# Optimization experiments

Measured on AMD Instinct MI355X. Metric: run time of the kernel, lower is better.

The kernel has to match this reference:

```python
import jax, jax.numpy as jnp
import numpy as np

EMB, HEADS = 1024, 16
B, T = 4, 1024

def setup_inputs() -> dict:
    key = jax.random.key(0)
    ks = jax.random.split(key, 6)
    sc = 1.0 / np.sqrt(EMB)
    return {
        "x": jax.random.normal(ks[0], (B, T, EMB), jnp.float32),
        "Wq": jax.random.normal(ks[1], (EMB, EMB), jnp.float32) * sc,
        "Wk": jax.random.normal(ks[2], (EMB, EMB), jnp.float32) * sc,
        "Wv": jax.random.normal(ks[3], (EMB, EMB), jnp.float32) * sc,
        "Wo": jax.random.normal(ks[4], (EMB, EMB), jnp.float32) * sc,
        "bo": jnp.zeros((EMB,), jnp.float32),
    }

def reference(x, Wq, Wk, Wv, Wo, bo):
    b, t, e = x.shape
    h = HEADS
    s = e // h
    # nn.Linear(emb, emb, bias=False): y = x @ W.T
    q = (x @ Wq.T).reshape(b, t, h, s).transpose(0, 2, 1, 3)  # (b,h,t,s)
    k = (x @ Wk.T).reshape(b, t, h, s).transpose(0, 2, 1, 3)
    v = (x @ Wv.T).reshape(b, t, h, s).transpose(0, 2, 1, 3)
    scale = e ** 0.25  # original scales q and k each by emb**(1/4)
    q = q / scale
    k = k / scale
    dot = jnp.einsum('bhqs,bhks->bhqk', q, k)  # (b,h,t,t)
    # causal mask: strict upper triangle -> -inf (mask_diagonal=False)
    causal = jnp.tril(jnp.ones((t, t), dtype=bool))
    dot = jnp.where(causal[None, None], dot, -jnp.inf)
    attn = jax.nn.softmax(dot, axis=-1)
    out = jnp.einsum('bhqk,bhks->bhqs', attn, v)  # (b,h,t,s)
    out = out.transpose(0, 2, 1, 3).reshape(b, t, e)
    return out @ Wo.T + bo
```

## Files before the change

### kernel.cpp

```cpp
#include <hip/hip_runtime.h>
#include <hip/hip_bf16.h>
#include <stdint.h>


typedef __attribute__((ext_vector_type(8))) short short8;
typedef __attribute__((ext_vector_type(4))) float f32x4;
typedef __attribute__((ext_vector_type(16))) float f32x16;

__device__ __forceinline__ unsigned short f2bf(float f) {
    union { float f; unsigned int u; } v; v.f = f;
    unsigned int r = v.u + 0x7FFFu + ((v.u >> 16) & 1u);
    return (unsigned short)(r >> 16);
}

__device__ __forceinline__ void gload_lds16(const ushort* g, ushort* l) {
    __builtin_amdgcn_global_load_lds(
        (const __attribute__((address_space(1))) void*)g,
        (__attribute__((address_space(3))) void*)l,
        16, 0, 0);
}

__device__ __forceinline__ void wait_vmcnt_0() { asm volatile("s_waitcnt vmcnt(0)" ::: "memory"); }
__device__ __forceinline__ void wait_vmcnt_3() { asm volatile("s_waitcnt vmcnt(3)" ::: "memory"); }
__device__ __forceinline__ void wait_vmcnt_4() { asm volatile("s_waitcnt vmcnt(4)" ::: "memory"); }

__device__ __forceinline__ void block_barrier() {
    __builtin_amdgcn_sched_barrier(0);
    __builtin_amdgcn_s_barrier();
    __builtin_amdgcn_sched_barrier(0);
}
__device__ __forceinline__ void lgk0() {
    asm volatile("s_waitcnt lgkmcnt(0)" ::: "memory");
    __builtin_amdgcn_sched_barrier(0);
}

__device__ __forceinline__ unsigned int cvtpk(float lo, float hi) {
    unsigned int r;
    asm("v_cvt_pk_bf16_f32 %0, %1, %2" : "=v"(r) : "v"(lo), "v"(hi));
    return r;
}
__device__ __forceinline__ void plswap(unsigned int& x, unsigned int& y) {
    asm volatile("v_permlane32_swap_b32 %0, %1" : "+v"(x), "+v"(y));
}

__global__ __launch_bounds__(256) void cast_bf16(
    const float* __restrict__ x,  const float* __restrict__ wq,
    const float* __restrict__ wk, const float* __restrict__ wv,
    const float* __restrict__ wo, ushort* __restrict__ dst)
{
    size_t e0 = (size_t)(blockIdx.x * 256 + threadIdx.x) * 4;
    const float* src; size_t off;
    if      (e0 < 4194304u) { src = x;  off = e0; }
    else if (e0 < 5242880u) { src = wq; off = e0 - 4194304u; }
    else if (e0 < 6291456u) { src = wk; off = e0 - 5242880u; }
    else if (e0 < 7340032u) { src = wv; off = e0 - 6291456u; }
    else                    { src = wo; off = e0 - 7340032u; }
    float4 v = *(const float4*)(src + off);
    ushort4 o;
    o.x = f2bf(v.x); o.y = f2bf(v.y); o.z = f2bf(v.z); o.w = f2bf(v.w);
    *(ushort4*)(dst + e0) = o;
}

__global__ __launch_bounds__(512) void gemm_qkv_8ph(
    const ushort* __restrict__ A, const ushort* __restrict__ B,
    ushort* __restrict__ Qb, ushort* __restrict__ Kb, ushort* __restrict__ Vtb)
{
    __shared__ ushort lds[2][2][2][128 * 64];

    const int id = blockIdx.x;
    const int swz = (id & 7) * 24 + (id >> 3);
    const int bx = swz % 12, by = swz / 12;
    const int n0 = bx * 256, m0 = by * 256;
    const int t = threadIdx.x, w = t >> 6, l = t & 63;
    const int l15 = l & 15, l4 = l >> 4;
    const int wr = w >> 2, wc = w & 3;
    const int K = 1024;

    auto stage_half = [&](const ushort* gsrc, ushort* dst) {
        #pragma unroll
        for (int i = 0; i < 2; ++i) {
            int slot = i * 512 + t;
            int r = slot >> 3, blk = slot & 7;
            gload_lds16(gsrc + (size_t)r * K + ((blk ^ (r & 7)) << 3),
                        dst + (i * 512 + w * 64) * 8);
        }
    };
    auto stageA = [&](int kt, int h, int buf) {
        stage_half(A + (size_t)(m0 + h * 128) * K + kt * 64, &lds[buf][0][h][0]);
    };
    auto stageB = [&](int kt, int h, int buf) {
        stage_half(B + (size_t)(n0 + h * 128) * K + kt * 64, &lds[buf][1][h][0]);
    };

    short8 af[8];
    short8 vb0[4], vb1[4];
    f32x4 acc[8][4] = {};

    auto readA = [&](int buf, int qm) {
        const ushort* base = &lds[buf][0][wr][0];
        #pragma unroll
        for (int kk = 0; kk < 2; ++kk)
            #pragma unroll
            for (int mt = 0; mt < 4; ++mt) {
                int row = qm * 64 + mt * 16 + l15;
                af[kk * 4 + mt] = *(const short8*)
                    &base[row * 64 + (((kk * 4 + l4) ^ (row & 7)) << 3)];
            }
    };
    auto readB0 = [&](int buf, int qn) {
        const ushort* base = &lds[buf][1][wc >> 1][0];
        #pragma unroll
        for (int kk = 0; kk < 2; ++kk)
            #pragma unroll
            for (int nt = 0; nt < 2; ++nt) {
                int row = (wc & 1) * 64 + qn * 32 + nt * 16 + l15;
                vb0[kk * 2 + nt] = *(const short8*)
                    &base[row * 64 + (((kk * 4 + l4) ^ (row & 7)) << 3)];
            }
    };
    auto readB1 = [&](int buf, int qn) {
        const ushort* base = &lds[buf][1][wc >> 1][0];
        #pragma unroll
        for (int kk = 0; kk < 2; ++kk)
            #pragma unroll
            for (int nt = 0; nt < 2; ++nt) {
                int row = (wc & 1) * 64 + qn * 32 + nt * 16 + l15;
                vb1[kk * 2 + nt] = *(const short8*)
                    &base[row * 64 + (((kk * 4 + l4) ^ (row & 7)) << 3)];
            }
    };
    auto mfma_vb0 = [&](int qm, int qn) {
        __builtin_amdgcn_s_setprio(1);
        #pragma unroll
        for (int kk = 0; kk < 2; ++kk)
            #pragma unroll
            for (int mt = 0; mt < 4; ++mt)
                #pragma unroll
                for (int nt = 0; nt < 2; ++nt)
                    acc[qm * 4 + mt][qn * 2 + nt] =
                        __builtin_amdgcn_mfma_f32_16x16x32_bf16(
                            af[kk * 4 + mt], vb0[kk * 2 + nt],
                            acc[qm * 4 + mt][qn * 2 + nt], 0, 0, 0);
        __builtin_amdgcn_s_setprio(0);
    };
    auto mfma_vb1 = [&](int qm, int qn) {
        __builtin_amdgcn_s_setprio(1);
        #pragma unroll
        for (int kk = 0; kk < 2; ++kk)
            #pragma unroll
            for (int mt = 0; mt < 4; ++mt)
                #pragma unroll
                for (int nt = 0; nt < 2; ++nt)
                    acc[qm * 4 + mt][qn * 2 + nt] =
                        __builtin_amdgcn_mfma_f32_16x16x32_bf16(
                            af[kk * 4 + mt], vb1[kk * 2 + nt],
                            acc[qm * 4 + mt][qn * 2 + nt], 0, 0, 0);
        __builtin_amdgcn_s_setprio(0);
    };

    stageB(0, 0, 0); stageB(0, 1, 0); stageA(0, 0, 0); stageA(0, 1, 0);
    stageB(1, 0, 1); stageB(1, 1, 1);
    wait_vmcnt_4();
    block_barrier();

    for (int j = 0; j < 8; ++j) {
        const bool more = (j < 7);
        readA(0, 0); readB0(0, 0);
        stageA(2 * j + 1, 0, 1);
        block_barrier(); lgk0();
        mfma_vb0(0, 0);
        block_barrier();
        readB1(0, 1);
        stageA(2 * j + 1, 1, 1);
        block_barrier(); lgk0();
        mfma_vb1(0, 1);
        block_barrier();
        readA(0, 1);
        if (more) stageB(2 * j + 2, 0, 0);
        block_barrier(); lgk0();
        mfma_vb1(1, 1);
        block_barrier();
        if (more) stageB(2 * j + 2, 1, 0);
        block_barrier(); lgk0();
        mfma_vb0(1, 0);
        if (more) wait_vmcnt_4(); else wait_vmcnt_0();
        block_barrier();
        readA(1, 0); readB0(1, 0);
        if (more) stageA(2 * j + 2, 0, 0);
        block_barrier(); lgk0();
        mfma_vb0(0, 0);
        block_barrier();
        readB1(1, 1);
        if (more) stageA(2 * j + 2, 1, 0);
        block_barrier(); lgk0();
        mfma_vb1(0, 1);
        block_barrier();
        readA(1, 1);
        if (more) stageB(2 * j + 3, 0, 1);
        block_barrier(); lgk0();
        mfma_vb1(1, 1);
        block_barrier();
        if (more) stageB(2 * j + 3, 1, 1);
        block_barrier(); lgk0();
        mfma_vb0(1, 0);
        if (more) { wait_vmcnt_4(); block_barrier(); }
    }

    #pragma unroll
    for (int qm = 0; qm < 2; ++qm) {
        #pragma unroll
        for (int mt = 0; mt < 4; ++mt) {
            int row = m0 + wr * 128 + qm * 64 + mt * 16 + l4 * 4;
            int b = row >> 10, tq = row & 1023;
            #pragma unroll
            for (int qn = 0; qn < 2; ++qn) {
                #pragma unroll
                for (int nt = 0; nt < 2; ++nt) {
                    int col = n0 + wc * 64 + qn * 32 + nt * 16 + l15;
                    int sel = col >> 10;
                    int cw  = col & 1023;
                    int h = cw >> 6, s = cw & 63;
                    f32x4 v = acc[qm * 4 + mt][qn * 2 + nt];
                    if (sel == 2) {
                        ushort4 o;
                        o.x = f2bf(v[0]); o.y = f2bf(v[1]);
                        o.z = f2bf(v[2]); o.w = f2bf(v[3]);
                        *(ushort4*)&Vtb[(((size_t)(b * 16 + h)) * 64 + s) * 1024 + tq] = o;
                    } else {
                        ushort* dst = (sel == 0) ? Qb : Kb;
                        float scl = (sel == 0) ? 0.03125f : 1.0f;
                        #pragma unroll
                        for (int jj = 0; jj < 4; ++jj)
                            dst[(((size_t)(b * 16 + h)) * 1024 + tq + jj) * 64 + s] =
                                f2bf(v[jj] * scl);
                    }
                }
            }
        }
    }
}

template<int MODE, int BM, int WRg, int WCg>
__global__ __launch_bounds__(256) void gemm_bt(
    const ushort* __restrict__ A, const ushort* __restrict__ B,
    float* __restrict__ Cout, const float* __restrict__ bias)
{
    constexpr int MF = BM / (32 * WRg);
    constexpr int NF = 128 / (32 * WCg);
    constexpr int NSTEP = 32;
    const int K = 1024;
    const int n0 = blockIdx.x * 128;
    const int m0 = blockIdx.y * BM;
    const int t  = threadIdx.x;
    const int w  = t >> 6, l = t & 63;
    const int l31 = l & 31, lh = l >> 5;
    const int wr = w / WCg, wc = w % WCg;

    __shared__ ushort As[3 * BM * 32];
    __shared__ ushort Bs[3 * 128 * 32];

    auto stage = [&](int j) {
        const int buf = j % 3;
        const int k0 = j * 32;
        #pragma unroll
        for (int i = 0; i < BM / 64; ++i) {
            int slot = i * 256 + t;
            int r = slot >> 2, blk = slot & 3;
            gload_lds16(A + (size_t)(m0 + r) * K + k0 + ((blk ^ ((r >> 1) & 3)) << 3),
                        &As[buf * BM * 32 + (i * 256 + w * 64) * 8]);
        }
        #pragma unroll
        for (int i = 0; i < 2; ++i) {
            int slot = i * 256 + t;
            int r = slot >> 2, blk = slot & 3;
            gload_lds16(B + (size_t)(n0 + r) * K + k0 + ((blk ^ ((r >> 1) & 3)) << 3),
                        &Bs[buf * 128 * 32 + (i * 256 + w * 64) * 8]);
        }
    };

    f32x16 acc[MF][NF] = {};

    stage(0); stage(1);
    for (int kt = 0; kt < NSTEP; ++kt) {
        if (kt < NSTEP - 1) { if (BM == 128) wait_vmcnt_4(); else wait_vmcnt_3(); }
        else wait_vmcnt_0();
        block_barrier();
        if (kt + 2 < NSTEP) stage(kt + 2);

        const ushort* Ab = &As[(kt % 3) * BM * 32];
        const ushort* Bb = &Bs[(kt % 3) * 128 * 32];
        #pragma unroll
        for (int kk = 0; kk < 2; ++kk) {
            const int c = kk * 2 + lh;
            short8 af[MF], bf[NF];
            #pragma unroll
            for (int mt = 0; mt < MF; ++mt) {
                int row = wr * (MF * 32) + mt * 32 + l31;
                af[mt] = *(const short8*)&Ab[row * 32 + ((c ^ ((row >> 1) & 3)) << 3)];
            }
            #pragma unroll
            for (int nt = 0; nt < NF; ++nt) {
                int row = wc * (NF * 32) + nt * 32 + l31;
                bf[nt] = *(const short8*)&Bb[row * 32 + ((c ^ ((row >> 1) & 3)) << 3)];
            }
            #pragma unroll
            for (int mt = 0; mt < MF; ++mt)
                #pragma unroll
                for (int nt = 0; nt < NF; ++nt)
                    acc[mt][nt] = __builtin_amdgcn_mfma_f32_32x32x16_bf16(
                        af[mt], bf[nt], acc[mt][nt], 0, 0, 0);
        }
    }

    #pragma unroll
    for (int mt = 0; mt < MF; ++mt) {
        int rbase = m0 + wr * (MF * 32) + mt * 32 + 4 * lh;
        #pragma unroll
        for (int nt = 0; nt < NF; ++nt) {
            int col = n0 + wc * (NF * 32) + nt * 32 + l31;
            float bi = bias[col];
            #pragma unroll
            for (int reg = 0; reg < 16; ++reg) {
                int row = rbase + (reg & 3) + 8 * (reg >> 2);
                Cout[(size_t)row * 1024 + col] = acc[mt][nt][reg] + bi;
            }
        }
    }
}

#define PVSTEP(SF, B, VK0, VK1)                                               \
    {                                                                         \
        unsigned int A0_ = cvtpk(SF[(B) + 0], SF[(B) + 1]);                   \
        unsigned int A1_ = cvtpk(SF[(B) + 2], SF[(B) + 3]);                   \
        unsigned int B0_ = cvtpk(SF[(B) + 4], SF[(B) + 5]);                   \
        unsigned int B1_ = cvtpk(SF[(B) + 6], SF[(B) + 7]);                   \
        plswap(A0_, B0_);                                                     \
        plswap(A1_, B1_);                                                     \
        union { unsigned int u[4]; short8 s; } pa_;                           \
        pa_.u[0] = A0_; pa_.u[1] = A1_; pa_.u[2] = B0_; pa_.u[3] = B1_;       \
        accO0 = __builtin_amdgcn_mfma_f32_32x32x16_bf16(pa_.s, VK0, accO0, 0, 0, 0); \
        accO1 = __builtin_amdgcn_mfma_f32_32x32x16_bf16(pa_.s, VK1, accO1, 0, 0, 0); \
    }

#define EXP4(SF, R)                                                           \
    SF[(R) + 0] = __expf(SF[(R) + 0]); ls0 += SF[(R) + 0];                    \
    SF[(R) + 1] = __expf(SF[(R) + 1]); ls1 += SF[(R) + 1];                    \
    SF[(R) + 2] = __expf(SF[(R) + 2]); ls2 += SF[(R) + 2];                    \
    SF[(R) + 3] = __expf(SF[(R) + 3]); ls3 += SF[(R) + 3];

#define MEXP1(SF, R, OFF, LS)                                                 \
    {                                                                         \
        int kv_ = (OFF) + ((R) & 3) + 8 * ((R) >> 2) + 4 * hi;                \
        float e_ = (kv_ > qrow) ? 0.f : __expf(SF[R]);                        \
        SF[R] = e_; LS += e_;                                                 \
    }

#define MEXP16(SF, OFF)                                                       \
    MEXP1(SF, 0, OFF, ls0)  MEXP1(SF, 1, OFF, ls1)                            \
    MEXP1(SF, 2, OFF, ls2)  MEXP1(SF, 3, OFF, ls3)                            \
    MEXP1(SF, 4, OFF, ls0)  MEXP1(SF, 5, OFF, ls1)                            \
    MEXP1(SF, 6, OFF, ls2)  MEXP1(SF, 7, OFF, ls3)                            \
    MEXP1(SF, 8, OFF, ls0)  MEXP1(SF, 9, OFF, ls1)                            \
    MEXP1(SF, 10, OFF, ls2) MEXP1(SF, 11, OFF, ls3)                           \
    MEXP1(SF, 12, OFF, ls0) MEXP1(SF, 13, OFF, ls1)                           \
    MEXP1(SF, 14, OFF, ls2) MEXP1(SF, 15, OFF, ls3)

__global__ __launch_bounds__(64, 2) void attn_kernel(
    const ushort* __restrict__ Q, const ushort* __restrict__ Kp,
    const ushort* __restrict__ Vt, ushort* __restrict__ O)
{
    const int id = blockIdx.x;
    const int bh = id & 63;
    const int g  = 31 - (id >> 6);
    const int l = threadIdx.x;
    const int l31 = l & 31, hi = l >> 5;

    const ushort* Qbase = Q + ((size_t)bh * 1024 + (size_t)g * 32) * 64;
    const ushort* Kr0 = Kp + (size_t)bh * 65536 + (size_t)l31 * 64 + hi * 8;
    const ushort* Kr1 = Kr0 + 32 * 64;
    const ushort* Vr0 = Vt + (size_t)bh * 65536 + (size_t)l31 * 1024 + hi * 8;
    const ushort* Vr1 = Vr0 + 32 * 1024;

    short8 qb0 = *(const short8*)(Qbase + (size_t)l31 * 64 +  0 + hi * 8);
    short8 qb1 = *(const short8*)(Qbase + (size_t)l31 * 64 + 16 + hi * 8);
    short8 qb2 = *(const short8*)(Qbase + (size_t)l31 * 64 + 32 + hi * 8);
    short8 qb3 = *(const short8*)(Qbase + (size_t)l31 * 64 + 48 + hi * 8);

    f32x16 accO0 = {}, accO1 = {};
    float ls0 = 0.f, ls1 = 0.f, ls2 = 0.f, ls3 = 0.f;
    const int qrow = g * 32 + l31;
    const int nkv = (g >> 1) + 1;

    for (int kvt = 0; kvt < nkv - 1; ++kvt) {
        const ushort* kp0 = Kr0 + (size_t)kvt * 4096;
        const ushort* kp1 = Kr1 + (size_t)kvt * 4096;
        const ushort* vp0 = Vr0 + kvt * 64;
        const ushort* vp1 = Vr1 + kvt * 64;
        short8 k00 = *(const short8*)(kp0);
        short8 k01 = *(const short8*)(kp0 + 16);
        short8 k02 = *(const short8*)(kp0 + 32);
        short8 k03 = *(const short8*)(kp0 + 48);
        short8 k10 = *(const short8*)(kp1);
        short8 k11 = *(const short8*)(kp1 + 16);
        short8 k12 = *(const short8*)(kp1 + 32);
        short8 k13 = *(const short8*)(kp1 + 48);
        short8 v00 = *(const short8*)(vp0);
        short8 v01 = *(const short8*)(vp0 + 16);
        short8 v02 = *(const short8*)(vp0 + 32);
        short8 v03 = *(const short8*)(vp0 + 48);
        short8 v10 = *(const short8*)(vp1);
        short8 v11 = *(const short8*)(vp1 + 16);
        short8 v12 = *(const short8*)(vp1 + 32);
        short8 v13 = *(const short8*)(vp1 + 48);
        __builtin_amdgcn_sched_barrier(0);

        f32x16 sf0 = {}, sf1 = {};
        sf0 = __builtin_amdgcn_mfma_f32_32x32x16_bf16(k00, qb0, sf0, 0, 0, 0);
        sf0 = __builtin_amdgcn_mfma_f32_32x32x16_bf16(k01, qb1, sf0, 0, 0, 0);
        sf0 = __builtin_amdgcn_mfma_f32_32x32x16_bf16(k02, qb2, sf0, 0, 0, 0);
        sf0 = __builtin_amdgcn_mfma_f32_32x32x16_bf16(k03, qb3, sf0, 0, 0, 0);
        sf1 = __builtin_amdgcn_mfma_f32_32x32x16_bf16(k10, qb0, sf1, 0, 0, 0);
        sf1 = __builtin_amdgcn_mfma_f32_32x32x16_bf16(k11, qb1, sf1, 0, 0, 0);
        sf1 = __builtin_amdgcn_mfma_f32_32x32x16_bf16(k12, qb2, sf1, 0, 0, 0);
        sf1 = __builtin_amdgcn_mfma_f32_32x32x16_bf16(k13, qb3, sf1, 0, 0, 0);

        EXP4(sf0, 0) EXP4(sf0, 4) EXP4(sf0, 8) EXP4(sf0, 12)
        EXP4(sf1, 0) EXP4(sf1, 4) EXP4(sf1, 8) EXP4(sf1, 12)

        PVSTEP(sf0, 0, v00, v10)
        PVSTEP(sf0, 8, v01, v11)
        PVSTEP(sf1, 0, v02, v12)
        PVSTEP(sf1, 8, v03, v13)
    }

    {
        const int kvb = (nkv - 1) * 64;
        const ushort* kp0 = Kr0 + (size_t)(nkv - 1) * 4096;
        const ushort* vp0 = Vr0 + (nkv - 1) * 64;
        const ushort* vp1 = Vr1 + (nkv - 1) * 64;
        short8 k00 = *(const short8*)(kp0);
        short8 k01 = *(const short8*)(kp0 + 16);
        short8 k02 = *(const short8*)(kp0 + 32);
        short8 k03 = *(const short8*)(kp0 + 48);
        short8 v00 = *(const short8*)(vp0);
        short8 v01 = *(const short8*)(vp0 + 16);
        short8 v02 = *(const short8*)(vp0 + 32);
        short8 v03 = *(const short8*)(vp0 + 48);
        short8 v10 = *(const short8*)(vp1);
        short8 v11 = *(const short8*)(vp1 + 16);
        short8 v12 = *(const short8*)(vp1 + 32);
        short8 v13 = *(const short8*)(vp1 + 48);
        __builtin_amdgcn_sched_barrier(0);

        f32x16 sf0 = {};
        sf0 = __builtin_amdgcn_mfma_f32_32x32x16_bf16(k00, qb0, sf0, 0, 0, 0);
        sf0 = __builtin_amdgcn_mfma_f32_32x32x16_bf16(k01, qb1, sf0, 0, 0, 0);
        sf0 = __builtin_amdgcn_mfma_f32_32x32x16_bf16(k02, qb2, sf0, 0, 0, 0);
        sf0 = __builtin_amdgcn_mfma_f32_32x32x16_bf16(k03, qb3, sf0, 0, 0, 0);
        MEXP16(sf0, kvb)
        PVSTEP(sf0, 0, v00, v10)
        PVSTEP(sf0, 8, v01, v11)

        if (g & 1) {
            const ushort* kp1 = Kr1 + (size_t)(nkv - 1) * 4096;
            short8 k10 = *(const short8*)(kp1);
            short8 k11 = *(const short8*)(kp1 + 16);
            short8 k12 = *(const short8*)(kp1 + 32);
            short8 k13 = *(const short8*)(kp1 + 48);
            f32x16 sf1 = {};
            sf1 = __builtin_amdgcn_mfma_f32_32x32x16_bf16(k10, qb0, sf1, 0, 0, 0);
            sf1 = __builtin_amdgcn_mfma_f32_32x32x16_bf16(k11, qb1, sf1, 0, 0, 0);
            sf1 = __builtin_amdgcn_mfma_f32_32x32x16_bf16(k12, qb2, sf1, 0, 0, 0);
            sf1 = __builtin_amdgcn_mfma_f32_32x32x16_bf16(k13, qb3, sf1, 0, 0, 0);
            MEXP16(sf1, kvb + 32)
            PVSTEP(sf1, 0, v02, v12)
            PVSTEP(sf1, 8, v03, v13)
        }
    }

    float lsum = (ls0 + ls1) + (ls2 + ls3);
    float ltot = lsum + __shfl_xor(lsum, 32);
    float inv = 1.0f / ltot;
    const int b = bh >> 4, h = bh & 15;
    #pragma unroll
    for (int r = 0; r < 16; ++r) {
        int qr = (r & 3) + 8 * (r >> 2) + 4 * hi;
        float invr = __shfl(inv, qr);
        int tq = g * 32 + qr;
        O[((size_t)b * 1024 + tq) * 1024 + h * 64 + l31]      = f2bf(accO0[r] * invr);
        O[((size_t)b * 1024 + tq) * 1024 + h * 64 + 32 + l31] = f2bf(accO1[r] * invr);
    }
}

extern "C" void kernel_launch(void* const* d_in, const int* in_sizes, int n_in,
                              void* d_out, int out_size, void* d_ws, size_t ws_size,
                              hipStream_t stream) {
    const float* x  = (const float*)d_in[0];
    const float* wq = (const float*)d_in[1];
    const float* wk = (const float*)d_in[2];
    const float* wv = (const float*)d_in[3];
    const float* wo = (const float*)d_in[4];
    const float* bo = (const float*)d_in[5];
    float* out = (float*)d_out;

    ushort* ws  = (ushort*)d_ws;
    ushort* xb  = ws;
    ushort* wb  = ws + (4u << 20);
    ushort* Qb  = ws + (8u << 20);
    ushort* Kb  = ws + (12u << 20);
    ushort* Vtb = ws + (16u << 20);
    ushort* Ob  = ws + (20u << 20);

    cast_bf16<<<8192, 256, 0, stream>>>(x, wq, wk, wv, wo, ws);
    gemm_qkv_8ph<<<192, 512, 0, stream>>>(xb, wb, Qb, Kb, Vtb);
    attn_kernel<<<2048, 64, 0, stream>>>(Qb, Kb, Vtb, Ob);
    gemm_bt<1, 64, 1, 4><<<dim3(8, 64), 256, 0, stream>>>(
        Ob, wb + (3u << 20), out, bo);
}
```

Measured before the change: 104.2 us.

## Store Q/K/V in MFMA-fragment-ordered layout for contiguous attention loads

The QKV GEMM epilogue now writes Q, K and V into a tiled layout that matches the order in which the attention kernel's MFMA operands are consumed. Each wave's 16-byte per-lane loads then cover contiguous 1 KB chunks instead of strided rows. This is meant to cut memory transactions and improve coalescing in the attention kernel, which reads K and V repeatedly. In exchange, the GEMM epilogue stores become more scattered, especially the Q/K scalar stores.

```diff
diff --git a/kernel.cpp b/kernel.cpp
--- a/kernel.cpp
+++ b/kernel.cpp
@@ -63,7 +63,7 @@
 
 __global__ __launch_bounds__(512) void gemm_qkv_8ph(
     const ushort* __restrict__ A, const ushort* __restrict__ B,
-    ushort* __restrict__ Qb, ushort* __restrict__ Kb, ushort* __restrict__ Vtb)
+    ushort* __restrict__ Qf, ushort* __restrict__ Kf, ushort* __restrict__ Vf)
 {
     __shared__ ushort lds[2][2][2][128 * 64];
 
@@ -211,7 +211,7 @@
         #pragma unroll
         for (int mt = 0; mt < 4; ++mt) {
             int row = m0 + wr * 128 + qm * 64 + mt * 16 + l4 * 4;
-            int b = row >> 10, tq = row & 1023;
+            int b = row >> 10, tok = row & 1023;
             #pragma unroll
             for (int qn = 0; qn < 2; ++qn) {
                 #pragma unroll
@@ -220,19 +220,24 @@
                     int sel = col >> 10;
                     int cw  = col & 1023;
                     int h = cw >> 6, s = cw & 63;
+                    size_t bhb = (size_t)(b * 16 + h) * 65536;
                     f32x4 v = acc[qm * 4 + mt][qn * 2 + nt];
                     if (sel == 2) {
+                        size_t off = bhb + (tok >> 6) * 4096 + (s >> 5) * 2048
+                                   + ((tok >> 4) & 3) * 512 + ((tok >> 3) & 1) * 256
+                                   + (s & 31) * 8 + (tok & 7);
                         ushort4 o;
                         o.x = f2bf(v[0]); o.y = f2bf(v[1]);
                         o.z = f2bf(v[2]); o.w = f2bf(v[3]);
-                        *(ushort4*)&Vtb[(((size_t)(b * 16 + h)) * 64 + s) * 1024 + tq] = o;
+                        *(ushort4*)&Vf[off] = o;
                     } else {
-                        ushort* dst = (sel == 0) ? Qb : Kb;
+                        ushort* dst = (sel == 0) ? Qf : Kf;
                         float scl = (sel == 0) ? 0.03125f : 1.0f;
+                        size_t off = bhb + (tok >> 5) * 2048 + (s >> 4) * 512
+                                   + ((s >> 3) & 1) * 256 + (tok & 31) * 8 + (s & 7);
                         #pragma unroll
                         for (int jj = 0; jj < 4; ++jj)
-                            dst[(((size_t)(b * 16 + h)) * 1024 + tq + jj) * 64 + s] =
-                                f2bf(v[jj] * scl);
+                            dst[off + jj * 8] = f2bf(v[jj] * scl);
                     }
                 }
             }
@@ -366,8 +371,8 @@
     MEXP1(SF, 14, OFF, ls2) MEXP1(SF, 15, OFF, ls3)
 
 __global__ __launch_bounds__(64, 2) void attn_kernel(
-    const ushort* __restrict__ Q, const ushort* __restrict__ Kp,
-    const ushort* __restrict__ Vt, ushort* __restrict__ O)
+    const ushort* __restrict__ Qf, const ushort* __restrict__ Kf,
+    const ushort* __restrict__ Vf, ushort* __restrict__ O)
 {
     const int id = blockIdx.x;
     const int bh = id & 63;
@@ -375,16 +380,14 @@
     const int l = threadIdx.x;
     const int l31 = l & 31, hi = l >> 5;
 
-    const ushort* Qbase = Q + ((size_t)bh * 1024 + (size_t)g * 32) * 64;
-    const ushort* Kr0 = Kp + (size_t)bh * 65536 + (size_t)l31 * 64 + hi * 8;
-    const ushort* Kr1 = Kr0 + 32 * 64;
-    const ushort* Vr0 = Vt + (size_t)bh * 65536 + (size_t)l31 * 1024 + hi * 8;
-    const ushort* Vr1 = Vr0 + 32 * 1024;
-
-    short8 qb0 = *(const short8*)(Qbase + (size_t)l31 * 64 +  0 + hi * 8);
-    short8 qb1 = *(const short8*)(Qbase + (size_t)l31 * 64 + 16 + hi * 8);
-    short8 qb2 = *(const short8*)(Qbase + (size_t)l31 * 64 + 32 + hi * 8);
-    short8 qb3 = *(const short8*)(Qbase + (size_t)l31 * 64 + 48 + hi * 8);
+    const ushort* qp = Qf + (size_t)bh * 65536 + (size_t)g * 2048 + (size_t)l * 8;
+    const ushort* kp = Kf + (size_t)bh * 65536 + (size_t)l * 8;
+    const ushort* vp = Vf + (size_t)bh * 65536 + (size_t)l * 8;
+
+    short8 qb0 = *(const short8*)(qp);
+    short8 qb1 = *(const short8*)(qp + 512);
+    short8 qb2 = *(const short8*)(qp + 1024);
+    short8 qb3 = *(const short8*)(qp + 1536);
 
     f32x16 accO0 = {}, accO1 = {};
     float ls0 = 0.f, ls1 = 0.f, ls2 = 0.f, ls3 = 0.f;
@@ -392,26 +395,24 @@
     const int nkv = (g >> 1) + 1;
 
     for (int kvt = 0; kvt < nkv - 1; ++kvt) {
-        const ushort* kp0 = Kr0 + (size_t)kvt * 4096;
-        const ushort* kp1 = Kr1 + (size_t)kvt * 4096;
-        const ushort* vp0 = Vr0 + kvt * 64;
-        const ushort* vp1 = Vr1 + kvt * 64;
-        short8 k00 = *(const short8*)(kp0);
-        short8 k01 = *(const short8*)(kp0 + 16);
-        short8 k02 = *(const short8*)(kp0 + 32);
-        short8 k03 = *(const short8*)(kp0 + 48);
-        short8 k10 = *(const short8*)(kp1);
-        short8 k11 = *(const short8*)(kp1 + 16);
-        short8 k12 = *(const short8*)(kp1 + 32);
-        short8 k13 = *(const short8*)(kp1 + 48);
-        short8 v00 = *(const short8*)(vp0);
-        short8 v01 = *(const short8*)(vp0 + 16);
-        short8 v02 = *(const short8*)(vp0 + 32);
-        short8 v03 = *(const short8*)(vp0 + 48);
-        short8 v10 = *(const short8*)(vp1);
-        short8 v11 = *(const short8*)(vp1 + 16);
-        short8 v12 = *(const short8*)(vp1 + 32);
-        short8 v13 = *(const short8*)(vp1 + 48);
+        const ushort* kt = kp + (size_t)kvt * 4096;
+        const ushort* vt = vp + (size_t)kvt * 4096;
+        short8 k00 = *(const short8*)(kt);
+        short8 k01 = *(const short8*)(kt + 512);
+        short8 k02 = *(const short8*)(kt + 1024);
+        short8 k03 = *(const short8*)(kt + 1536);
+        short8 k10 = *(const short8*)(kt + 2048);
+        short8 k11 = *(const short8*)(kt + 2560);
+        short8 k12 = *(const short8*)(kt + 3072);
+        short8 k13 = *(const short8*)(kt + 3584);
+        short8 v00 = *(const short8*)(vt);
+        short8 v01 = *(const short8*)(vt + 512);
+        short8 v02 = *(const short8*)(vt + 1024);
+        short8 v03 = *(const short8*)(vt + 1536);
+        short8 v10 = *(const short8*)(vt + 2048);
+        short8 v11 = *(const short8*)(vt + 2560);
+        short8 v12 = *(const short8*)(vt + 3072);
+        short8 v13 = *(const short8*)(vt + 3584);
         __builtin_amdgcn_sched_barrier(0);
 
         f32x16 sf0 = {}, sf1 = {};
@@ -435,21 +436,20 @@
 
     {
         const int kvb = (nkv - 1) * 64;
-        const ushort* kp0 = Kr0 + (size_t)(nkv - 1) * 4096;
-        const ushort* vp0 = Vr0 + (nkv - 1) * 64;
-        const ushort* vp1 = Vr1 + (nkv - 1) * 64;
-        short8 k00 = *(const short8*)(kp0);
-        short8 k01 = *(const short8*)(kp0 + 16);
-        short8 k02 = *(const short8*)(kp0 + 32);
-        short8 k03 = *(const short8*)(kp0 + 48);
-        short8 v00 = *(const short8*)(vp0);
-        short8 v01 = *(const short8*)(vp0 + 16);
-        short8 v02 = *(const short8*)(vp0 + 32);
-        short8 v03 = *(const short8*)(vp0 + 48);
-        short8 v10 = *(const short8*)(vp1);
-        short8 v11 = *(const short8*)(vp1 + 16);
-        short8 v12 = *(const short8*)(vp1 + 32);
-        short8 v13 = *(const short8*)(vp1 + 48);
+        const ushort* kt = kp + (size_t)(nkv - 1) * 4096;
+        const ushort* vt = vp + (size_t)(nkv - 1) * 4096;
+        short8 k00 = *(const short8*)(kt);
+        short8 k01 = *(const short8*)(kt + 512);
+        short8 k02 = *(const short8*)(kt + 1024);
+        short8 k03 = *(const short8*)(kt + 1536);
+        short8 v00 = *(const short8*)(vt);
+        short8 v01 = *(const short8*)(vt + 512);
+        short8 v02 = *(const short8*)(vt + 1024);
+        short8 v03 = *(const short8*)(vt + 1536);
+        short8 v10 = *(const short8*)(vt + 2048);
+        short8 v11 = *(const short8*)(vt + 2560);
+        short8 v12 = *(const short8*)(vt + 3072);
+        short8 v13 = *(const short8*)(vt + 3584);
         __builtin_amdgcn_sched_barrier(0);
 
         f32x16 sf0 = {};
@@ -462,11 +462,10 @@
         PVSTEP(sf0, 8, v01, v11)
 
         if (g & 1) {
-            const ushort* kp1 = Kr1 + (size_t)(nkv - 1) * 4096;
-            short8 k10 = *(const short8*)(kp1);
-            short8 k11 = *(const short8*)(kp1 + 16);
-            short8 k12 = *(const short8*)(kp1 + 32);
-            short8 k13 = *(const short8*)(kp1 + 48);
+            short8 k10 = *(const short8*)(kt + 2048);
+            short8 k11 = *(const short8*)(kt + 2560);
+            short8 k12 = *(const short8*)(kt + 3072);
+            short8 k13 = *(const short8*)(kt + 3584);
             f32x16 sf1 = {};
             sf1 = __builtin_amdgcn_mfma_f32_32x32x16_bf16(k10, qb0, sf1, 0, 0, 0);
             sf1 = __builtin_amdgcn_mfma_f32_32x32x16_bf16(k11, qb1, sf1, 0, 0, 0);
@@ -506,14 +505,14 @@
     ushort* ws  = (ushort*)d_ws;
     ushort* xb  = ws;
     ushort* wb  = ws + (4u << 20);
-    ushort* Qb  = ws + (8u << 20);
-    ushort* Kb  = ws + (12u << 20);
-    ushort* Vtb = ws + (16u << 20);
+    ushort* Qfb = ws + (8u << 20);
+    ushort* Kfb = ws + (12u << 20);
+    ushort* Vfb = ws + (16u << 20);
     ushort* Ob  = ws + (20u << 20);
 
     cast_bf16<<<8192, 256, 0, stream>>>(x, wq, wk, wv, wo, ws);
-    gemm_qkv_8ph<<<192, 512, 0, stream>>>(xb, wb, Qb, Kb, Vtb);
-    attn_kernel<<<2048, 64, 0, stream>>>(Qb, Kb, Vtb, Ob);
+    gemm_qkv_8ph<<<192, 512, 0, stream>>>(xb, wb, Qfb, Kfb, Vfb);
+    attn_kernel<<<2048, 64, 0, stream>>>(Qfb, Kfb, Vfb, Ob);
     gemm_bt<1, 64, 1, 4><<<dim3(8, 64), 256, 0, stream>>>(
         Ob, wb + (3u << 20), out, bo);
 }
```

New measurement: 84.98 us (median of 4 runs). 18.4% less time.
